# Kernel optimization log

Measured on AMD Instinct MI355X. Metric: run time of the kernel, lower is better.

## Reference

```python
import jax, jax.numpy as jnp
import numpy as np
import math

INPUTDIM = 256
OUTDIM = 512
GRIDSIZE = 64

def setup_inputs() -> dict:
    key = jax.random.key(0)
    k1, k2 = jax.random.split(key)
    x = jax.random.normal(k1, (4096, INPUTDIM), dtype=jnp.float32)
    # init: randn / (sqrt(inputdim) * sqrt(gridsize))  (smooth_initialization=False)
    fouriercoeffs = jax.random.normal(k2, (2, OUTDIM, INPUTDIM, GRIDSIZE), dtype=jnp.float32) / (
        math.sqrt(INPUTDIM) * math.sqrt(GRIDSIZE))
    bias = jnp.zeros((1, OUTDIM), dtype=jnp.float32)
    return {"x": x, "fouriercoeffs": fouriercoeffs, "bias": bias}

def reference(x, fouriercoeffs, bias):
    # x: [N, I]; fouriercoeffs: [2, O, I, G]; bias: [1, O]
    k = jnp.arange(1, GRIDSIZE + 1, dtype=x.dtype)          # [G]
    kx = x[:, :, None] * k[None, None, :]                   # [N, I, G]
    c = jnp.cos(kx)
    s = jnp.sin(kx)
    # contraction over (I, G) — GEMM-equivalent of the naive broadcast-sum
    y = jnp.einsum('nig,oig->no', c, fouriercoeffs[0])
    y = y + jnp.einsum('nig,oig->no', s, fouriercoeffs[1])
    y = y + bias
    return y
```

## Files before the change

### kernel.cpp

```cpp
#include <hip/hip_runtime.h>
#include <hip/hip_bf16.h>

#define IDIM 256
#define GDIM 64
#define ODIM 512
#define KD   (IDIM * GDIM)
#define TILE_SHORTS (512 * 64)
#define WS_NEED ((size_t)512 * TILE_SHORTS * 2)

typedef __attribute__((ext_vector_type(8))) short bhalf8;
typedef __attribute__((ext_vector_type(4))) float fvec4;
typedef __attribute__((ext_vector_type(4))) unsigned uvec4;

#define INV2PI 0.15915494309189535f

static __device__ __forceinline__ short bf16b(float v) {
    __hip_bfloat16 hb = __float2bfloat16(v);
    short s; __builtin_memcpy(&s, &hb, 2); return s;
}
static __device__ __forceinline__ unsigned cvtpk(float lo, float hi) {
    unsigned r;
    asm("v_cvt_pk_bf16_f32 %0, %1, %2" : "=v"(r) : "v"(lo), "v"(hi));
    return r;
}

__global__ void prep_b(const float* __restrict__ coeffs, short* __restrict__ ws) {
    const int b = blockIdx.x;
    const int i = b >> 1, h = b & 1;
    const int o = threadIdx.x;
    short* dst = ws + ((size_t)b * 512 + o) * 64;
    const int swz = (o & 7) << 4;
#pragma unroll
    for (int j = 0; j < 8; ++j) {
        const int z = j >> 2, Qq = j & 3;
        const float* src = coeffs + ((size_t)z * ODIM + o) * KD
                         + (size_t)i * GDIM + 16 * Qq + 8 * h;
        fvec4 v0 = ((const fvec4*)src)[0];
        fvec4 v1 = ((const fvec4*)src)[1];
        bhalf8 pk;
#pragma unroll
        for (int u = 0; u < 4; ++u) { pk[u] = bf16b(v0[u]); pk[4 + u] = bf16b(v1[u]); }
        *(bhalf8*)((char*)dst + ((j * 16) ^ swz)) = pk;
    }
}

__global__ void bias_init(const float* __restrict__ bias, float* __restrict__ out) {
    int idx = blockIdx.x * 256 + threadIdx.x;
    fvec4 bv = ((const fvec4*)bias)[idx & 127];
    ((fvec4*)out)[idx] = bv;
}

template<int USE_WS>
__global__ void __launch_bounds__(512, 2)
fkan_gemm(const float* __restrict__ x, const float* __restrict__ coeffs,
          const short* __restrict__ wsb, float* __restrict__ out) {
    __shared__ __align__(16) short B_lds[3][256 * 64];
    __shared__ float xl[256][33];

    const int bx = blockIdx.x;
    const int xcd = bx & 7, jj = bx >> 3;
    const int lg = xcd * 2 + (jj & 1);
    const int mt = jj >> 1;
    const int ot = lg >> 3, ks = lg & 7;
    const int row0 = mt * 256, col0 = ot * 256;
    const int i0 = ks * 32;

    const int t = threadIdx.x;
    const int lane = t & 63, wid = t >> 6;
    const int wave_m = wid & 1, wave_n = wid >> 1;

    const int rBb = wave_n * 64 + (lane & 15);
    const int kl  = (lane >> 4) * 16;
    const int msk = (lane & 7) << 4;
    const int rA0 = wave_m * 128 + (lane & 15);
    const float m0f = (float)(16 * (lane >> 4) + 1);

#pragma unroll
    for (int k2 = 0; k2 < 16; ++k2) {
        int idx = t + k2 * 512;
        int r = idx >> 5, c = idx & 31;
        xl[r][c] = x[(size_t)(row0 + r) * IDIM + i0 + c];
    }

    fvec4 acc[8][4];
#pragma unroll
    for (int a = 0; a < 8; ++a)
#pragma unroll
        for (int b = 0; b < 4; ++b) acc[a][b] = (fvec4)0.0f;

    auto dmaB = [&](int j) {
        const short* src = wsb + (size_t)(i0 * 2 + j) * TILE_SHORTS
                         + (size_t)col0 * 64 + (size_t)t * 8;
        const int bsel = j % 3;
#pragma unroll
        for (int q = 0; q < 4; ++q)
            __builtin_amdgcn_global_load_lds(
                (const __attribute__((address_space(1))) unsigned*)(src + q * 4096),
                (__attribute__((address_space(3))) unsigned*)
                    &B_lds[bsel][q * 4096 + wid * 512],
                16, 0, 0);
    };

    auto stage_fb = [&](int T) {
        const int bsel = T % 3;
        const int i = i0 + (T >> 1), hh = T & 1;
        const int o = t >> 1, z = t & 1;
        char* drow = (char*)&B_lds[bsel][o * 64];
        const int swz = (o & 7) << 4;
#pragma unroll
        for (int Qq = 0; Qq < 4; ++Qq) {
            const float* src = coeffs + ((size_t)z * ODIM + col0 + o) * KD
                             + (size_t)i * GDIM + 16 * Qq + 8 * hh;
            fvec4 v0 = ((const fvec4*)src)[0];
            fvec4 v1 = ((const fvec4*)src)[1];
            bhalf8 pk;
#pragma unroll
            for (int u = 0; u < 4; ++u) { pk[u] = bf16b(v0[u]); pk[4 + u] = bf16b(v1[u]); }
            *(bhalf8*)(drow + ((z * 64 + Qq * 16) ^ swz)) = pk;
        }
    };

    float stcA[8], stcB[8], stsA[8], stsB[8], stC2[8];

    if (USE_WS) {
        dmaB(0); dmaB(1);
        asm volatile("s_waitcnt vmcnt(4) lgkmcnt(0)" ::: "memory");
        __builtin_amdgcn_s_barrier();
    } else {
        __syncthreads();
    }

#pragma unroll 1
    for (int ii = 0; ii < 32; ++ii) {
#pragma unroll
        for (int h = 0; h < 2; ++h) {
            const int T = 2 * ii + h;
            const int bsel = T % 3;
            if (USE_WS) {
                int j = T + 2; if (j > 63) j = 63;
                dmaB(j);
                __builtin_amdgcn_sched_barrier(0);
            } else {
                stage_fb(T);
                __syncthreads();
            }

            const short* Bb = &B_lds[bsel][0];
            bhalf8 bq[4][2];
#pragma unroll
            for (int fn = 0; fn < 4; ++fn)
#pragma unroll
                for (int ksb = 0; ksb < 2; ++ksb)
                    bq[fn][ksb] = *(const bhalf8*)((const char*)Bb +
                        (size_t)(rBb + fn * 16) * 128 + ((ksb * 64 + kl) ^ msk));

#pragma unroll
            for (int hm = 0; hm < 2; ++hm) {
                unsigned pc[4][4], ps[4][4];
#pragma unroll
                for (int q2 = 0; q2 < 4; ++q2) {
                    const int r = hm * 4 + q2;
                    float cA, cB, sA, sB, C2;
                    if (h == 0) {
                        float xv = xl[rA0 + r * 16][ii];
                        float rev = xv * INV2PI;
                        float a0 = __builtin_amdgcn_fractf(rev * m0f);
                        float c0 = __builtin_amdgcn_cosf(a0);
                        float s0 = __builtin_amdgcn_sinf(a0);
                        float a1 = __builtin_amdgcn_fractf(rev);
                        float c1 = __builtin_amdgcn_cosf(a1);
                        float s1 = __builtin_amdgcn_sinf(a1);
                        C2 = c1 + c1;
                        cA = c0; sA = s0;
                        cB = c0 * c1 - s0 * s1;
                        sB = s0 * c1 + c0 * s1;
                        pc[q2][0] = cvtpk(cA, cB);
                        ps[q2][0] = cvtpk(sA, sB);
#pragma unroll
                        for (int p = 1; p < 4; ++p) {
                            float clo = __builtin_fmaf(C2, cB, -cA);
                            float slo = __builtin_fmaf(C2, sB, -sA);
                            cA = cB; cB = clo; sA = sB; sB = slo;
                            float chi = __builtin_fmaf(C2, cB, -cA);
                            float shi = __builtin_fmaf(C2, sB, -sA);
                            cA = cB; cB = chi; sA = sB; sB = shi;
                            pc[q2][p] = cvtpk(clo, chi);
                            ps[q2][p] = cvtpk(slo, shi);
                        }
                        stcA[r] = cA; stcB[r] = cB; stsA[r] = sA; stsB[r] = sB; stC2[r] = C2;
                    } else {
                        cA = stcA[r]; cB = stcB[r]; sA = stsA[r]; sB = stsB[r]; C2 = stC2[r];
#pragma unroll
                        for (int p = 0; p < 4; ++p) {
                            float clo = __builtin_fmaf(C2, cB, -cA);
                            float slo = __builtin_fmaf(C2, sB, -sA);
                            cA = cB; cB = clo; sA = sB; sB = slo;
                            float chi = __builtin_fmaf(C2, cB, -cA);
                            float shi = __builtin_fmaf(C2, sB, -sA);
                            cA = cB; cB = chi; sA = sB; sB = shi;
                            pc[q2][p] = cvtpk(clo, chi);
                            ps[q2][p] = cvtpk(slo, shi);
                        }
                    }
                }
                bhalf8 afc[4], afs[4];
#pragma unroll
                for (int q2 = 0; q2 < 4; ++q2) {
                    uvec4 uc = {pc[q2][0], pc[q2][1], pc[q2][2], pc[q2][3]};
                    uvec4 us = {ps[q2][0], ps[q2][1], ps[q2][2], ps[q2][3]};
                    afc[q2] = __builtin_bit_cast(bhalf8, uc);
                    afs[q2] = __builtin_bit_cast(bhalf8, us);
                }
#pragma unroll
                for (int q2 = 0; q2 < 4; ++q2)
#pragma unroll
                    for (int fn = 0; fn < 4; ++fn) {
                        acc[hm * 4 + q2][fn] = __builtin_amdgcn_mfma_f32_16x16x32_bf16(
                            afc[q2], bq[fn][0], acc[hm * 4 + q2][fn], 0, 0, 0);
                        acc[hm * 4 + q2][fn] = __builtin_amdgcn_mfma_f32_16x16x32_bf16(
                            afs[q2], bq[fn][1], acc[hm * 4 + q2][fn], 0, 0, 0);
                    }
            }

            if (USE_WS) {
                asm volatile("s_waitcnt vmcnt(4)" ::: "memory");
                __builtin_amdgcn_s_barrier();
            } else {
                __syncthreads();
            }
        }
    }

#pragma unroll
    for (int fm = 0; fm < 8; ++fm) {
#pragma unroll
        for (int fn = 0; fn < 4; ++fn) {
            int col = col0 + wave_n * 64 + fn * 16 + (lane & 15);
#pragma unroll
            for (int r = 0; r < 4; ++r) {
                int row = row0 + wave_m * 128 + fm * 16 + ((lane >> 4) * 4) + r;
                atomicAdd(&out[(size_t)row * ODIM + col], acc[fm][fn][r]);
            }
        }
    }
}

extern "C" void kernel_launch(void* const* d_in, const int* in_sizes, int n_in,
                              void* d_out, int out_size, void* d_ws, size_t ws_size,
                              hipStream_t stream) {
    (void)in_sizes; (void)n_in; (void)out_size;
    const float* x      = (const float*)d_in[0];
    const float* coeffs = (const float*)d_in[1];
    const float* bias   = (const float*)d_in[2];
    float* out = (float*)d_out;

    const bool use_ws = (ws_size >= WS_NEED) && (((uintptr_t)d_ws & 15) == 0);

    bias_init<<<dim3(2048), dim3(256), 0, stream>>>(bias, out);
    if (use_ws) {
        prep_b<<<dim3(512), dim3(512), 0, stream>>>(coeffs, (short*)d_ws);
        fkan_gemm<1><<<dim3(256), dim3(512), 0, stream>>>(x, coeffs, (const short*)d_ws, out);
    } else {
        fkan_gemm<0><<<dim3(256), dim3(512), 0, stream>>>(x, coeffs, nullptr, out);
    }
}
```

Before: 206.0 us.

## Shrink GEMM tiles to 128x128 with 256-thread blocks and LDS-staged base angles

Halves the block tile to 128x128 with 4 waves per block, launches 1024 blocks at an occupancy target of 4 per CU, and drops the B pipeline from three LDS buffers to two. Per-row base angles and their cos/sin are now computed once per 4-column chunk and stored in LDS. The cos and sin fragments are built in two separate phases, each followed by its MFMA batch under raised wave priority. The aim is more resident waves and lower per-thread register use, to hide the transcendental and MFMA latency. In exchange, every step now waits with vmcnt(0) plus a full barrier, so the previous prefetch-depth overlap is lost, and the smaller tiles reuse A and B less.

```diff
diff --git a/kernel.cpp b/kernel.cpp
--- a/kernel.cpp
+++ b/kernel.cpp
@@ -50,19 +50,24 @@
     ((fvec4*)out)[idx] = bv;
 }
 
+#define FENCE() do { asm volatile("s_waitcnt vmcnt(0) lgkmcnt(0)" ::: "memory"); \
+                     __builtin_amdgcn_sched_barrier(0); \
+                     __syncthreads(); } while (0)
+
 template<int USE_WS>
-__global__ void __launch_bounds__(512, 2)
+__global__ void __launch_bounds__(256, 4)
 fkan_gemm(const float* __restrict__ x, const float* __restrict__ coeffs,
           const short* __restrict__ wsb, float* __restrict__ out) {
-    __shared__ __align__(16) short B_lds[3][256 * 64];
-    __shared__ float xl[256][33];
+    __shared__ __align__(16) short B_lds[2][128 * 64];
+    __shared__ float  sl_rev[4][128];
+    __shared__ float2 sl_cs[4][128];
 
     const int bx = blockIdx.x;
-    const int xcd = bx & 7, jj = bx >> 3;
-    const int lg = xcd * 2 + (jj & 1);
-    const int mt = jj >> 1;
-    const int ot = lg >> 3, ks = lg & 7;
-    const int row0 = mt * 256, col0 = ot * 256;
+    const int xcd = bx & 7, j = bx >> 3;
+    const int lg  = xcd * 4 + (j & 3);
+    const int mt  = j >> 2;
+    const int ot  = lg >> 3, ks = lg & 7;
+    const int row0 = mt * 128, col0 = ot * 128;
     const int i0 = ks * 32;
 
     const int t = threadIdx.x;
@@ -72,38 +77,47 @@
     const int rBb = wave_n * 64 + (lane & 15);
     const int kl  = (lane >> 4) * 16;
     const int msk = (lane & 7) << 4;
-    const int rA0 = wave_m * 128 + (lane & 15);
-    const float m0f = (float)(16 * (lane >> 4) + 1);
-
-#pragma unroll
-    for (int k2 = 0; k2 < 16; ++k2) {
-        int idx = t + k2 * 512;
-        int r = idx >> 5, c = idx & 31;
-        xl[r][c] = x[(size_t)(row0 + r) * IDIM + i0 + c];
-    }
-
-    fvec4 acc[8][4];
-#pragma unroll
-    for (int a = 0; a < 8; ++a)
+    const int rA0 = wave_m * 64 + (lane & 15);
+    const float m0base = (float)(16 * (lane >> 4) + 1);
+
+    fvec4 acc[4][4];
+#pragma unroll
+    for (int a = 0; a < 4; ++a)
 #pragma unroll
         for (int b = 0; b < 4; ++b) acc[a][b] = (fvec4)0.0f;
 
-    auto dmaB = [&](int j) {
-        const short* src = wsb + (size_t)(i0 * 2 + j) * TILE_SHORTS
+    auto fill_sl = [&](int chunk) {
+#pragma unroll
+        for (int w = 0; w < 2; ++w) {
+            int idx = t + w * 256;
+            int il2 = idx & 3, r2 = idx >> 2;
+            float xv = x[(size_t)(row0 + r2) * IDIM + i0 + chunk * 4 + il2];
+            float rev = xv * INV2PI;
+            float a = __builtin_amdgcn_fractf(rev);
+            float2 cs;
+            cs.x = __builtin_amdgcn_cosf(a);
+            cs.y = __builtin_amdgcn_sinf(a);
+            sl_rev[il2][r2] = rev;
+            sl_cs[il2][r2] = cs;
+        }
+    };
+
+    auto dmaB = [&](int T1) {
+        const short* src = wsb + (size_t)(i0 * 2 + T1) * TILE_SHORTS
                          + (size_t)col0 * 64 + (size_t)t * 8;
-        const int bsel = j % 3;
+        const int bsel = T1 & 1;
 #pragma unroll
         for (int q = 0; q < 4; ++q)
             __builtin_amdgcn_global_load_lds(
-                (const __attribute__((address_space(1))) unsigned*)(src + q * 4096),
+                (const __attribute__((address_space(1))) unsigned*)(src + q * 2048),
                 (__attribute__((address_space(3))) unsigned*)
-                    &B_lds[bsel][q * 4096 + wid * 512],
+                    &B_lds[bsel][q * 2048 + wid * 512],
                 16, 0, 0);
     };
 
-    auto stage_fb = [&](int T) {
-        const int bsel = T % 3;
-        const int i = i0 + (T >> 1), hh = T & 1;
+    auto stage_fb = [&](int T1) {
+        const int bsel = T1 & 1;
+        const int i = i0 + (T1 >> 1), hh = T1 & 1;
         const int o = t >> 1, z = t & 1;
         char* drow = (char*)&B_lds[bsel][o * 64];
         const int swz = (o & 7) << 4;
@@ -120,125 +134,112 @@
         }
     };
 
-    float stcA[8], stcB[8], stsA[8], stsB[8], stC2[8];
-
-    if (USE_WS) {
-        dmaB(0); dmaB(1);
-        asm volatile("s_waitcnt vmcnt(4) lgkmcnt(0)" ::: "memory");
-        __builtin_amdgcn_s_barrier();
-    } else {
-        __syncthreads();
-    }
+    fill_sl(0);
+    if (USE_WS) dmaB(0);
+    FENCE();
 
 #pragma unroll 1
-    for (int ii = 0; ii < 32; ++ii) {
-#pragma unroll
-        for (int h = 0; h < 2; ++h) {
-            const int T = 2 * ii + h;
-            const int bsel = T % 3;
-            if (USE_WS) {
-                int j = T + 2; if (j > 63) j = 63;
-                dmaB(j);
-                __builtin_amdgcn_sched_barrier(0);
-            } else {
-                stage_fb(T);
-                __syncthreads();
+    for (int T = 0; T < 64; ++T) {
+        if ((T & 7) == 0 && T > 0) {
+            fill_sl(T >> 3);
+            FENCE();
+        }
+        if (USE_WS) {
+            if (T < 63) dmaB(T + 1);
+            __builtin_amdgcn_sched_barrier(0);
+        } else {
+            stage_fb(T);
+            FENCE();
+        }
+
+        const int bsel = T & 1;
+        const int il = (T >> 1) & 3;
+        const float m0h = m0base + (float)((T & 1) * 8);
+        const short* Bb = &B_lds[bsel][0];
+
+        float c_sA[4], c_sB[4], c_C2[4];
+        bhalf8 afc[4];
+#pragma unroll
+        for (int fm = 0; fm < 4; ++fm) {
+            const int rr = rA0 + fm * 16;
+            float rev = sl_rev[il][rr];
+            float2 cs1 = sl_cs[il][rr];
+            float C2 = cs1.x + cs1.x;
+            float a0 = __builtin_amdgcn_fractf(rev * m0h);
+            float c0 = __builtin_amdgcn_cosf(a0);
+            float s0 = __builtin_amdgcn_sinf(a0);
+            float cA = c0;
+            float cB = __builtin_fmaf(c0, cs1.x, -(s0 * cs1.y));
+            float sB = __builtin_fmaf(s0, cs1.x,  (c0 * cs1.y));
+            c_sA[fm] = s0; c_sB[fm] = sB; c_C2[fm] = C2;
+            uvec4 uc;
+            uc[0] = cvtpk(cA, cB);
+#pragma unroll
+            for (int p = 1; p < 4; ++p) {
+                float cn = __builtin_fmaf(C2, cB, -cA); cA = cB; cB = cn;
+                cn = __builtin_fmaf(C2, cB, -cA); cA = cB; cB = cn;
+                uc[p] = cvtpk(cA, cB);
             }
-
-            const short* Bb = &B_lds[bsel][0];
-            bhalf8 bq[4][2];
+            afc[fm] = __builtin_bit_cast(bhalf8, uc);
+        }
+        {
+            bhalf8 bq[4];
 #pragma unroll
             for (int fn = 0; fn < 4; ++fn)
-#pragma unroll
-                for (int ksb = 0; ksb < 2; ++ksb)
-                    bq[fn][ksb] = *(const bhalf8*)((const char*)Bb +
-                        (size_t)(rBb + fn * 16) * 128 + ((ksb * 64 + kl) ^ msk));
-
-#pragma unroll
-            for (int hm = 0; hm < 2; ++hm) {
-                unsigned pc[4][4], ps[4][4];
-#pragma unroll
-                for (int q2 = 0; q2 < 4; ++q2) {
-                    const int r = hm * 4 + q2;
-                    float cA, cB, sA, sB, C2;
-                    if (h == 0) {
-                        float xv = xl[rA0 + r * 16][ii];
-                        float rev = xv * INV2PI;
-                        float a0 = __builtin_amdgcn_fractf(rev * m0f);
-                        float c0 = __builtin_amdgcn_cosf(a0);
-                        float s0 = __builtin_amdgcn_sinf(a0);
-                        float a1 = __builtin_amdgcn_fractf(rev);
-                        float c1 = __builtin_amdgcn_cosf(a1);
-                        float s1 = __builtin_amdgcn_sinf(a1);
-                        C2 = c1 + c1;
-                        cA = c0; sA = s0;
-                        cB = c0 * c1 - s0 * s1;
-                        sB = s0 * c1 + c0 * s1;
-                        pc[q2][0] = cvtpk(cA, cB);
-                        ps[q2][0] = cvtpk(sA, sB);
-#pragma unroll
-                        for (int p = 1; p < 4; ++p) {
-                            float clo = __builtin_fmaf(C2, cB, -cA);
-                            float slo = __builtin_fmaf(C2, sB, -sA);
-                            cA = cB; cB = clo; sA = sB; sB = slo;
-                            float chi = __builtin_fmaf(C2, cB, -cA);
-                            float shi = __builtin_fmaf(C2, sB, -sA);
-                            cA = cB; cB = chi; sA = sB; sB = shi;
-                            pc[q2][p] = cvtpk(clo, chi);
-                            ps[q2][p] = cvtpk(slo, shi);
-                        }
-                        stcA[r] = cA; stcB[r] = cB; stsA[r] = sA; stsB[r] = sB; stC2[r] = C2;
-                    } else {
-                        cA = stcA[r]; cB = stcB[r]; sA = stsA[r]; sB = stsB[r]; C2 = stC2[r];
-#pragma unroll
-                        for (int p = 0; p < 4; ++p) {
-                            float clo = __builtin_fmaf(C2, cB, -cA);
-                            float slo = __builtin_fmaf(C2, sB, -sA);
-                            cA = cB; cB = clo; sA = sB; sB = slo;
-                            float chi = __builtin_fmaf(C2, cB, -cA);
-                            float shi = __builtin_fmaf(C2, sB, -sA);
-                            cA = cB; cB = chi; sA = sB; sB = shi;
-                            pc[q2][p] = cvtpk(clo, chi);
-                            ps[q2][p] = cvtpk(slo, shi);
-                        }
-                    }
-                }
-                bhalf8 afc[4], afs[4];
-#pragma unroll
-                for (int q2 = 0; q2 < 4; ++q2) {
-                    uvec4 uc = {pc[q2][0], pc[q2][1], pc[q2][2], pc[q2][3]};
-                    uvec4 us = {ps[q2][0], ps[q2][1], ps[q2][2], ps[q2][3]};
-                    afc[q2] = __builtin_bit_cast(bhalf8, uc);
-                    afs[q2] = __builtin_bit_cast(bhalf8, us);
-                }
-#pragma unroll
-                for (int q2 = 0; q2 < 4; ++q2)
-#pragma unroll
-                    for (int fn = 0; fn < 4; ++fn) {
-                        acc[hm * 4 + q2][fn] = __builtin_amdgcn_mfma_f32_16x16x32_bf16(
-                            afc[q2], bq[fn][0], acc[hm * 4 + q2][fn], 0, 0, 0);
-                        acc[hm * 4 + q2][fn] = __builtin_amdgcn_mfma_f32_16x16x32_bf16(
-                            afs[q2], bq[fn][1], acc[hm * 4 + q2][fn], 0, 0, 0);
-                    }
+                bq[fn] = *(const bhalf8*)((const char*)Bb +
+                    (size_t)(rBb + fn * 16) * 128 + (kl ^ msk));
+            __builtin_amdgcn_s_setprio(1);
+#pragma unroll
+            for (int fm = 0; fm < 4; ++fm)
+#pragma unroll
+                for (int fn = 0; fn < 4; ++fn)
+                    acc[fm][fn] = __builtin_amdgcn_mfma_f32_16x16x32_bf16(
+                        afc[fm], bq[fn], acc[fm][fn], 0, 0, 0);
+            __builtin_amdgcn_s_setprio(0);
+        }
+
+        bhalf8 afs[4];
+#pragma unroll
+        for (int fm = 0; fm < 4; ++fm) {
+            float C2 = c_C2[fm];
+            float sA = c_sA[fm], sB = c_sB[fm];
+            uvec4 us;
+            us[0] = cvtpk(sA, sB);
+#pragma unroll
+            for (int p = 1; p < 4; ++p) {
+                float sn = __builtin_fmaf(C2, sB, -sA); sA = sB; sB = sn;
+                sn = __builtin_fmaf(C2, sB, -sA); sA = sB; sB = sn;
+                us[p] = cvtpk(sA, sB);
             }
-
-            if (USE_WS) {
-                asm volatile("s_waitcnt vmcnt(4)" ::: "memory");
-                __builtin_amdgcn_s_barrier();
-            } else {
-                __syncthreads();
-            }
-        }
-    }
-
-#pragma unroll
-    for (int fm = 0; fm < 8; ++fm) {
+            afs[fm] = __builtin_bit_cast(bhalf8, us);
+        }
+        {
+            bhalf8 bq[4];
+#pragma unroll
+            for (int fn = 0; fn < 4; ++fn)
+                bq[fn] = *(const bhalf8*)((const char*)Bb +
+                    (size_t)(rBb + fn * 16) * 128 + ((64 + kl) ^ msk));
+            __builtin_amdgcn_s_setprio(1);
+#pragma unroll
+            for (int fm = 0; fm < 4; ++fm)
+#pragma unroll
+                for (int fn = 0; fn < 4; ++fn)
+                    acc[fm][fn] = __builtin_amdgcn_mfma_f32_16x16x32_bf16(
+                        afs[fm], bq[fn], acc[fm][fn], 0, 0, 0);
+            __builtin_amdgcn_s_setprio(0);
+        }
+
+        FENCE();
+    }
+
+#pragma unroll
+    for (int fm = 0; fm < 4; ++fm) {
 #pragma unroll
         for (int fn = 0; fn < 4; ++fn) {
             int col = col0 + wave_n * 64 + fn * 16 + (lane & 15);
 #pragma unroll
             for (int r = 0; r < 4; ++r) {
-                int row = row0 + wave_m * 128 + fm * 16 + ((lane >> 4) * 4) + r;
+                int row = row0 + wave_m * 64 + fm * 16 + ((lane >> 4) * 4) + r;
                 atomicAdd(&out[(size_t)row * ODIM + col], acc[fm][fn][r]);
             }
         }
@@ -259,8 +260,8 @@
     bias_init<<<dim3(2048), dim3(256), 0, stream>>>(bias, out);
     if (use_ws) {
         prep_b<<<dim3(512), dim3(512), 0, stream>>>(coeffs, (short*)d_ws);
-        fkan_gemm<1><<<dim3(256), dim3(512), 0, stream>>>(x, coeffs, (const short*)d_ws, out);
+        fkan_gemm<1><<<dim3(1024), dim3(256), 0, stream>>>(x, coeffs, (const short*)d_ws, out);
     } else {
-        fkan_gemm<0><<<dim3(256), dim3(512), 0, stream>>>(x, coeffs, nullptr, out);
-    }
-}
+        fkan_gemm<0><<<dim3(1024), dim3(256), 0, stream>>>(x, coeffs, nullptr, out);
+    }
+}
```

New measurement: 196.3 us. -4.7%, faster.
